# Kernel optimization log

Measured on AMD Instinct MI355X. Metric: run time of the kernel, lower is better.

The kernel has to match this reference:

```python
import jax, jax.numpy as jnp
import numpy as np

V, E, NH, NL, FF, MAXLEN = 32000, 512, 8, 4, 2048, 80
B, L = 32, 80
EPS = 1e-5


def _ln(x, w, b):
    m = jnp.mean(x, axis=-1, keepdims=True)
    v = jnp.var(x, axis=-1, keepdims=True)
    return (x - m) / jnp.sqrt(v + EPS) * w + b


def _mha(q_in, kv_in, in_w, in_b, out_w, out_b, mask):
    # in_w: [3E, E] packed q/k/v like torch MultiheadAttention
    Bq, Lq, Em = q_in.shape
    Lk = kv_in.shape[1]
    hd = Em // NH
    q = q_in @ in_w[:Em].T + in_b[:Em]
    k = kv_in @ in_w[Em:2 * Em].T + in_b[Em:2 * Em]
    v = kv_in @ in_w[2 * Em:].T + in_b[2 * Em:]
    q = q.reshape(Bq, Lq, NH, hd).transpose(0, 2, 1, 3)
    k = k.reshape(Bq, Lk, NH, hd).transpose(0, 2, 1, 3)
    v = v.reshape(Bq, Lk, NH, hd).transpose(0, 2, 1, 3)
    s = jnp.einsum('bhqd,bhkd->bhqk', q, k) * (1.0 / float(np.sqrt(hd)))
    if mask is not None:
        s = s + mask
    a = jax.nn.softmax(s, axis=-1)
    o = jnp.einsum('bhqk,bhkd->bhqd', a, v).transpose(0, 2, 1, 3).reshape(Bq, Lq, Em)
    return o @ out_w.T + out_b


def _forward(caps, W_in, b_in, pos_emb, sa_in_w, sa_in_b, sa_out_w, sa_out_b,
             ca_in_w, ca_in_b, ca_out_w, ca_out_b, ff1_w, ff1_b, ff2_w, ff2_b,
             ln1_w, ln1_b, ln2_w, ln2_b, ln3_w, ln3_b, out_w, out_b):
    Bc, Lc = caps.shape
    # one-hot encode then dense Linear(vocab -> emb): semantically an embedding gather
    oh = jax.nn.one_hot(caps, V, dtype=jnp.float32)          # [B, L, V]
    x = oh @ W_in.T + b_in + pos_emb[:Lc][None]               # [B, L, E]
    mask = jnp.where(jnp.triu(jnp.ones((Lc, Lc), bool), 1), -jnp.inf, 0.0).astype(jnp.float32)
    mem = jnp.zeros((Bc, 1, E), jnp.float32)
    for i in range(NL):  # post-norm TransformerDecoderLayer (torch default, relu FFN)
        sa = _mha(x, x, sa_in_w[i], sa_in_b[i], sa_out_w[i], sa_out_b[i], mask)
        x = _ln(x + sa, ln1_w[i], ln1_b[i])
        ca = _mha(x, mem, ca_in_w[i], ca_in_b[i], ca_out_w[i], ca_out_b[i], None)
        x = _ln(x + ca, ln2_w[i], ln2_b[i])
        ff = jax.nn.relu(x @ ff1_w[i].T + ff1_b[i]) @ ff2_w[i].T + ff2_b[i]
        x = _ln(x + ff, ln3_w[i], ln3_b[i])
    return x @ out_w.T + out_b                                # [B, L, V]


def setup_inputs() -> dict:
    key = jax.random.key(0)
    ks = jax.random.split(key, 16)
    g = lambda k, shape, s=0.02: jax.random.normal(k, shape, jnp.float32) * s
    caps = jax.random.randint(ks[0], (B, L), 1, V)  # avoid pad_idx=0
    return {
        'caps': caps,
        'W_in': g(ks[1], (E, V)),
        'b_in': jnp.zeros((E,), jnp.float32),
        'pos_emb': g(ks[2], (MAXLEN, E)),
        'sa_in_w': g(ks[3], (NL, 3 * E, E)),
        'sa_in_b': jnp.zeros((NL, 3 * E), jnp.float32),
        'sa_out_w': g(ks[4], (NL, E, E)),
        'sa_out_b': jnp.zeros((NL, E), jnp.float32),
        'ca_in_w': g(ks[5], (NL, 3 * E, E)),
        'ca_in_b': jnp.zeros((NL, 3 * E), jnp.float32),
        'ca_out_w': g(ks[6], (NL, E, E)),
        'ca_out_b': jnp.zeros((NL, E), jnp.float32),
        'ff1_w': g(ks[7], (NL, FF, E)),
        'ff1_b': jnp.zeros((NL, FF), jnp.float32),
        'ff2_w': g(ks[8], (NL, E, FF)),
        'ff2_b': jnp.zeros((NL, E), jnp.float32),
        'ln1_w': jnp.ones((NL, E), jnp.float32),
        'ln1_b': jnp.zeros((NL, E), jnp.float32),
        'ln2_w': jnp.ones((NL, E), jnp.float32),
        'ln2_b': jnp.zeros((NL, E), jnp.float32),
        'ln3_w': jnp.ones((NL, E), jnp.float32),
        'ln3_b': jnp.zeros((NL, E), jnp.float32),
        'out_w': g(ks[9], (V, E)),
        'out_b': jnp.zeros((V,), jnp.float32),
    }


def reference(caps, W_in, b_in, pos_emb, sa_in_w, sa_in_b, sa_out_w, sa_out_b,
              ca_in_w, ca_in_b, ca_out_w, ca_out_b, ff1_w, ff1_b, ff2_w, ff2_b,
              ln1_w, ln1_b, ln2_w, ln2_b, ln3_w, ln3_b, out_w, out_b):
    return _forward(caps, W_in, b_in, pos_emb, sa_in_w, sa_in_b, sa_out_w, sa_out_b,
                    ca_in_w, ca_in_b, ca_out_w, ca_out_b, ff1_w, ff1_b, ff2_w, ff2_b,
                    ln1_w, ln1_b, ln2_w, ln2_b, ln3_w, ln3_b, out_w, out_b)
```

## Files before the change

kernel.cpp:

```cpp
#include <hip/hip_runtime.h>

typedef __attribute__((ext_vector_type(8))) short short8;
typedef __attribute__((ext_vector_type(4))) float floatx4;

__device__ __forceinline__ unsigned short f2bf(float f) {
  union { float f; unsigned int u; } un; un.f = f;
  unsigned int r = un.u + 0x7FFFu + ((un.u >> 16) & 1u);
  return (unsigned short)(r >> 16);
}
__device__ __forceinline__ float bf2f(unsigned short h) {
  union { unsigned int u; float f; } un; un.u = ((unsigned int)h) << 16;
  return un.f;
}

__device__ __forceinline__ void async_ld16(const unsigned short* g, unsigned short* l) {
  __builtin_amdgcn_global_load_lds(
      (const __attribute__((address_space(1))) void*)g,
      (__attribute__((address_space(3))) void*)l, 16, 0, 0);
}

template<int TM, int TN, int OUT_BF16, int RELU>
__global__ __launch_bounds__(256, (TM == 64) ? 4 : 2)
void gemm_bt(const unsigned short* __restrict__ A, const unsigned short* __restrict__ B,
             const float* __restrict__ bias, const float* __restrict__ res,
             void* __restrict__ Cout, int M, int N, int K) {
  constexpr int AELEM = TM * 64;
  constexpr int BELEM = TN * 64;
  constexpr int AIT = AELEM / 2048;
  constexpr int BIT = BELEM / 2048;
  constexpr int FM = TM / 32;
  constexpr int FN = TN / 32;
  __shared__ __align__(16) unsigned short sA[2][AELEM];
  __shared__ __align__(16) unsigned short sB[2][BELEM];
  const int tid = threadIdx.x;
  const int lane = tid & 63;
  const int wave = tid >> 6;
  const int m0 = blockIdx.x * TM;
  const int n0 = blockIdx.y * TN;

  int a_off[AIT], b_off[BIT], lb[AIT > BIT ? AIT : BIT];
#pragma unroll
  for (int it = 0; it < AIT; it++) {
    int e = it * 2048 + tid * 8;
    int r = e >> 6, cb = (e >> 3) & 7;
    a_off[it] = (m0 + r) * K + ((cb ^ (r & 7)) * 8);
    lb[it] = it * 2048 + wave * 512;
  }
#pragma unroll
  for (int it = 0; it < BIT; it++) {
    int e = it * 2048 + tid * 8;
    int r = e >> 6, cb = (e >> 3) & 7;
    b_off[it] = (n0 + r) * K + ((cb ^ (r & 7)) * 8);
  }

  floatx4 acc[FM][FN];
#pragma unroll
  for (int i = 0; i < FM; i++)
#pragma unroll
    for (int j = 0; j < FN; j++) acc[i][j] = (floatx4){0.f, 0.f, 0.f, 0.f};

  const int nkt = K >> 6;
  const int wm = (wave >> 1) * (TM / 2);
  const int wn = (wave & 1) * (TN / 2);
  const int fr = lane & 15;
  const int q = lane >> 4;

  auto stage = [&](int kt, int buf) {
    const int k0 = kt << 6;
#pragma unroll
    for (int it = 0; it < AIT; it++) async_ld16(A + (size_t)a_off[it] + k0, &sA[buf][lb[it]]);
#pragma unroll
    for (int it = 0; it < BIT; it++) async_ld16(B + (size_t)b_off[it] + k0, &sB[buf][lb[it]]);
  };

  stage(0, 0);
  for (int kt = 0; kt < nkt; kt++) {
    __syncthreads();
    if (kt + 1 < nkt) stage(kt + 1, (kt + 1) & 1);
    const unsigned short* pA = sA[kt & 1];
    const unsigned short* pB = sB[kt & 1];
#pragma unroll
    for (int kk = 0; kk < 64; kk += 32) {
      short8 af[FM], bfr[FN];
      const int cba = (kk >> 3) + q;
#pragma unroll
      for (int t = 0; t < FM; t++) {
        int ra = wm + t * 16 + fr;
        af[t] = *(const short8*)&pA[ra * 64 + ((cba ^ (ra & 7)) * 8)];
      }
#pragma unroll
      for (int t = 0; t < FN; t++) {
        int rb = wn + t * 16 + fr;
        bfr[t] = *(const short8*)&pB[rb * 64 + ((cba ^ (rb & 7)) * 8)];
      }
#pragma unroll
      for (int i = 0; i < FM; i++)
#pragma unroll
        for (int j = 0; j < FN; j++)
          acc[i][j] = __builtin_amdgcn_mfma_f32_16x16x32_bf16(af[i], bfr[j], acc[i][j], 0, 0, 0);
    }
  }

#pragma unroll
  for (int i = 0; i < FM; i++) {
#pragma unroll
    for (int j = 0; j < FN; j++) {
#pragma unroll
      for (int rg = 0; rg < 4; rg++) {
        int row = m0 + wm + i * 16 + q * 4 + rg;
        int col = n0 + wn + j * 16 + fr;
        float v = acc[i][j][rg];
        if (bias) v += bias[col];
        if (res)  v += res[(size_t)row * N + col];
        if (RELU) v = v > 0.f ? v : 0.f;
        if (OUT_BF16) ((unsigned short*)Cout)[(size_t)row * N + col] = f2bf(v);
        else          ((float*)Cout)[(size_t)row * N + col] = v;
      }
    }
  }
}

__global__ __launch_bounds__(512)
void embed_kernel(const int* __restrict__ caps, const float* __restrict__ W_in,
                  const float* __restrict__ b_in, const float* __restrict__ pos,
                  float* __restrict__ x, unsigned short* __restrict__ xbf) {
  int pidx = blockIdx.x;
  int l = pidx % 80;
  int tok = caps[pidx];
  int e = threadIdx.x;
  float v = W_in[(size_t)e * 32000 + tok] + b_in[e] + pos[l * 512 + e];
  x[(size_t)pidx * 512 + e] = v;
  xbf[(size_t)pidx * 512 + e] = f2bf(v);
}

__global__ __launch_bounds__(256)
void ln_kernel(const float* __restrict__ in, const float* __restrict__ w,
               const float* __restrict__ b, float* __restrict__ xout,
               unsigned short* __restrict__ xbf) {
  int row = blockIdx.x * 4 + (threadIdx.x >> 6);
  int lane = threadIdx.x & 63;
  const float* p = in + (size_t)row * 512;
  float vals[8];
  float s = 0.f, s2 = 0.f;
#pragma unroll
  for (int j = 0; j < 8; j++) {
    float t = p[lane + j * 64];
    vals[j] = t; s += t; s2 += t * t;
  }
#pragma unroll
  for (int off = 32; off; off >>= 1) { s += __shfl_xor(s, off); s2 += __shfl_xor(s2, off); }
  float mean = s * (1.f / 512.f);
  float inv = rsqrtf(s2 * (1.f / 512.f) - mean * mean + 1e-5f);
#pragma unroll
  for (int j = 0; j < 8; j++) {
    int c = lane + j * 64;
    float y = (vals[j] - mean) * inv * w[c] + b[c];
    xout[(size_t)row * 512 + c] = y;
    xbf[(size_t)row * 512 + c] = f2bf(y);
  }
}

__global__ __launch_bounds__(256)
void ln2x_kernel(const float* __restrict__ in, const float* __restrict__ cav,
                 const float* __restrict__ w1, const float* __restrict__ b1,
                 const float* __restrict__ w2, const float* __restrict__ b2,
                 float* __restrict__ xout, unsigned short* __restrict__ xbf) {
  int row = blockIdx.x * 4 + (threadIdx.x >> 6);
  int lane = threadIdx.x & 63;
  const float* p = in + (size_t)row * 512;
  float vals[8];
  float s = 0.f, s2 = 0.f;
#pragma unroll
  for (int j = 0; j < 8; j++) {
    float t = p[lane + j * 64];
    vals[j] = t; s += t; s2 += t * t;
  }
#pragma unroll
  for (int off = 32; off; off >>= 1) { s += __shfl_xor(s, off); s2 += __shfl_xor(s2, off); }
  float mean = s * (1.f / 512.f);
  float inv = rsqrtf(s2 * (1.f / 512.f) - mean * mean + 1e-5f);
  float s_b = 0.f, s2_b = 0.f;
#pragma unroll
  for (int j = 0; j < 8; j++) {
    int c = lane + j * 64;
    float y = (vals[j] - mean) * inv * w1[c] + b1[c] + cav[c];
    vals[j] = y; s_b += y; s2_b += y * y;
  }
#pragma unroll
  for (int off = 32; off; off >>= 1) { s_b += __shfl_xor(s_b, off); s2_b += __shfl_xor(s2_b, off); }
  float mean2 = s_b * (1.f / 512.f);
  float inv2 = rsqrtf(s2_b * (1.f / 512.f) - mean2 * mean2 + 1e-5f);
#pragma unroll
  for (int j = 0; j < 8; j++) {
    int c = lane + j * 64;
    float y = (vals[j] - mean2) * inv2 * w2[c] + b2[c];
    xout[(size_t)row * 512 + c] = y;
    xbf[(size_t)row * 512 + c] = f2bf(y);
  }
}

__global__ __launch_bounds__(256)
void attn_kernel(const unsigned short* __restrict__ qkv, unsigned short* __restrict__ o) {
  __shared__ __align__(16) unsigned short sq[80][72];
  __shared__ __align__(16) unsigned short sk[80][72];
  __shared__ __align__(16) unsigned short svT[64][96];
  __shared__ __align__(16) unsigned short sp[80][96];
  __shared__ float ss[80][84];
  const int tid = threadIdx.x;
  const int lane = tid & 63;
  const int wave = tid >> 6;
  const int bb = blockIdx.x >> 3, hh = blockIdx.x & 7;
  const unsigned short* base = qkv + (size_t)bb * 80 * 1536 + hh * 64;

  for (int idx = tid; idx < 5120; idx += 256) {
    int r = idx >> 6, c = idx & 63;
    sq[r][c] = base[r * 1536 + c];
    sk[r][c] = base[r * 1536 + 512 + c];
    svT[c][r] = base[r * 1536 + 1024 + c];
  }
  for (int idx = tid; idx < 1024; idx += 256) svT[idx >> 4][80 + (idx & 15)] = 0;
  for (int idx = tid; idx < 1280; idx += 256) sp[idx >> 4][80 + (idx & 15)] = 0;
  __syncthreads();

  const int fr = lane & 15;
  const int q = lane >> 4;

  for (int t = wave; t < 25; t += 4) {
    int i0 = (t / 5) * 16, j0 = (t % 5) * 16;
    floatx4 acc = (floatx4){0.f, 0.f, 0.f, 0.f};
#pragma unroll
    for (int kk = 0; kk < 64; kk += 32) {
      short8 a = *(const short8*)&sq[i0 + fr][kk + q * 8];
      short8 b = *(const short8*)&sk[j0 + fr][kk + q * 8];
      acc = __builtin_amdgcn_mfma_f32_16x16x32_bf16(a, b, acc, 0, 0, 0);
    }
#pragma unroll
    for (int rg = 0; rg < 4; rg++) {
      int row = i0 + q * 4 + rg, col = j0 + fr;
      ss[row][col] = (col <= row) ? acc[rg] * 0.125f : -1e30f;
    }
  }
  __syncthreads();

  if (tid < 80) {
    float mx = -1e30f;
#pragma unroll
    for (int j = 0; j < 80; j++) mx = fmaxf(mx, ss[tid][j]);
    float sum = 0.f;
#pragma unroll
    for (int j = 0; j < 80; j++) { float e = __expf(ss[tid][j] - mx); ss[tid][j] = e; sum += e; }
    float inv = 1.f / sum;
#pragma unroll
    for (int j = 0; j < 80; j++) sp[tid][j] = f2bf(ss[tid][j] * inv);
  }
  __syncthreads();

  for (int t = wave; t < 20; t += 4) {
    int i0 = (t / 4) * 16, d0 = (t % 4) * 16;
    floatx4 acc = (floatx4){0.f, 0.f, 0.f, 0.f};
#pragma unroll
    for (int kk = 0; kk < 96; kk += 32) {
      short8 a = *(const short8*)&sp[i0 + fr][kk + q * 8];
      short8 b = *(const short8*)&svT[d0 + fr][kk + q * 8];
      acc = __builtin_amdgcn_mfma_f32_16x16x32_bf16(a, b, acc, 0, 0, 0);
    }
#pragma unroll
    for (int rg = 0; rg < 4; rg++) {
      int row = i0 + q * 4 + rg;
      o[((size_t)bb * 80 + row) * 512 + hh * 64 + d0 + fr] = f2bf(acc[rg]);
    }
  }
}

__global__ __launch_bounds__(256)
void cavec_kernel(const float* __restrict__ ca_out_w, const float* __restrict__ ca_in_b,
                  const float* __restrict__ ca_out_b, float* __restrict__ cav) {
  int g = blockIdx.x * 4 + (threadIdx.x >> 6);
  int lane = threadIdx.x & 63;
  int l = g >> 9, e = g & 511;
  const float* row = ca_out_w + ((size_t)l * 512 + e) * 512;
  const float* inb = ca_in_b + l * 1536 + 1024;
  float s = 0.f;
#pragma unroll
  for (int j = 0; j < 8; j++) s += row[lane + j * 64] * inb[lane + j * 64];
#pragma unroll
  for (int off = 32; off; off >>= 1) s += __shfl_xor(s, off);
  if (lane == 0) cav[g] = s + ca_out_b[l * 512 + e];
}

__global__ __launch_bounds__(256)
void convert_f2bf(const float* __restrict__ in, unsigned short* __restrict__ out, int n4) {
  int i = blockIdx.x * 256 + threadIdx.x;
  if (i < n4) {
    float4 v = ((const float4*)in)[i];
    ushort4 r;
    r.x = f2bf(v.x); r.y = f2bf(v.y); r.z = f2bf(v.z); r.w = f2bf(v.w);
    ((ushort4*)out)[i] = r;
  }
}

extern "C" void kernel_launch(void* const* d_in, const int* in_sizes, int n_in,
                              void* d_out, int out_size, void* d_ws, size_t ws_size,
                              hipStream_t stream) {
  const int*   caps     = (const int*)d_in[0];
  const float* W_in     = (const float*)d_in[1];
  const float* b_in     = (const float*)d_in[2];
  const float* pos_emb  = (const float*)d_in[3];
  const float* sa_in_w  = (const float*)d_in[4];
  const float* sa_in_b  = (const float*)d_in[5];
  const float* sa_out_w = (const float*)d_in[6];
  const float* sa_out_b = (const float*)d_in[7];
  const float* ca_in_b  = (const float*)d_in[9];
  const float* ca_out_w = (const float*)d_in[10];
  const float* ca_out_b = (const float*)d_in[11];
  const float* ff1_w    = (const float*)d_in[12];
  const float* ff1_b    = (const float*)d_in[13];
  const float* ff2_w    = (const float*)d_in[14];
  const float* ff2_b    = (const float*)d_in[15];
  const float* ln1_w    = (const float*)d_in[16];
  const float* ln1_b    = (const float*)d_in[17];
  const float* ln2_w    = (const float*)d_in[18];
  const float* ln2_b    = (const float*)d_in[19];
  const float* ln3_w    = (const float*)d_in[20];
  const float* ln3_b    = (const float*)d_in[21];
  const float* out_w    = (const float*)d_in[22];
  const float* out_b    = (const float*)d_in[23];

  char* ws = (char*)d_ws;
  size_t off = 0;
  auto alloc = [&](size_t bytes) {
    void* p = ws + off;
    off += (bytes + 255) & ~(size_t)255;
    return p;
  };
  unsigned short* w_sa_in  = (unsigned short*)alloc((size_t)4 * 1536 * 512 * 2);
  unsigned short* w_sa_out = (unsigned short*)alloc((size_t)4 * 512 * 512 * 2);
  unsigned short* w_ff1    = (unsigned short*)alloc((size_t)4 * 2048 * 512 * 2);
  unsigned short* w_ff2    = (unsigned short*)alloc((size_t)4 * 512 * 2048 * 2);
  unsigned short* w_out    = (unsigned short*)alloc((size_t)32000 * 512 * 2);
  float*          x        = (float*)alloc((size_t)2560 * 512 * 4);
  unsigned short* xbf      = (unsigned short*)alloc((size_t)2560 * 512 * 2);
  float*          t        = (float*)alloc((size_t)2560 * 512 * 4);
  unsigned short* qkv      = (unsigned short*)alloc((size_t)2560 * 1536 * 2);
  unsigned short* obf      = (unsigned short*)alloc((size_t)2560 * 512 * 2);
  unsigned short* hbf      = (unsigned short*)alloc((size_t)2560 * 2048 * 2);
  float*          cav      = (float*)alloc((size_t)2048 * 4);

  convert_f2bf<<<(786432 + 255) / 256, 256, 0, stream>>>(sa_in_w, w_sa_in, 786432);
  convert_f2bf<<<(262144 + 255) / 256, 256, 0, stream>>>(sa_out_w, w_sa_out, 262144);
  convert_f2bf<<<(1048576 + 255) / 256, 256, 0, stream>>>(ff1_w, w_ff1, 1048576);
  convert_f2bf<<<(1048576 + 255) / 256, 256, 0, stream>>>(ff2_w, w_ff2, 1048576);
  convert_f2bf<<<(4096000 + 255) / 256, 256, 0, stream>>>(out_w, w_out, 4096000);

  embed_kernel<<<2560, 512, 0, stream>>>(caps, W_in, b_in, pos_emb, x, xbf);
  cavec_kernel<<<512, 256, 0, stream>>>(ca_out_w, ca_in_b, ca_out_b, cav);

  for (int i = 0; i < 4; i++) {
    gemm_bt<128, 128, 1, 0><<<dim3(20, 12), 256, 0, stream>>>(
        xbf, w_sa_in + (size_t)i * 1536 * 512, sa_in_b + i * 1536, nullptr,
        qkv, 2560, 1536, 512);
    attn_kernel<<<256, 256, 0, stream>>>(qkv, obf);
    gemm_bt<64, 64, 0, 0><<<dim3(40, 8), 256, 0, stream>>>(
        obf, w_sa_out + (size_t)i * 512 * 512, sa_out_b + i * 512, x,
        t, 2560, 512, 512);
    ln2x_kernel<<<640, 256, 0, stream>>>(t, cav + i * 512,
        ln1_w + i * 512, ln1_b + i * 512, ln2_w + i * 512, ln2_b + i * 512, x, xbf);
    gemm_bt<128, 128, 1, 1><<<dim3(20, 16), 256, 0, stream>>>(
        xbf, w_ff1 + (size_t)i * 2048 * 512, ff1_b + i * 2048, nullptr,
        hbf, 2560, 2048, 512);
    gemm_bt<64, 64, 0, 0><<<dim3(40, 8), 256, 0, stream>>>(
        hbf, w_ff2 + (size_t)i * 512 * 2048, ff2_b + i * 512, x,
        t, 2560, 512, 2048);
    ln_kernel<<<640, 256, 0, stream>>>(t, ln3_w + i * 512, ln3_b + i * 512, x, xbf);
  }

  gemm_bt<128, 128, 0, 0><<<dim3(20, 250), 256, 0, stream>>>(
      xbf, w_out, out_b, nullptr, (float*)d_out, 2560, 32000, 512);
}
```

Measured before the change: 1.120 ms.

## Triple-buffer GEMM loads, remap blocks per XCD, nontemporal logits stores

The GEMM moves from double to triple buffering of LDS tiles. Explicit vmcnt waits and barriers let two future k-tiles be in flight while the current one is computed. Workgroup IDs are remapped so that consecutive tiles land on the same XCD for better L2 reuse. The large fp32 vocab projection output is written with nontemporal stores to avoid polluting cache. The cost is more LDS per block, and launch_bounds occupancy hints are lowered to match.

```diff
diff --git a/kernel.cpp b/kernel.cpp
--- a/kernel.cpp
+++ b/kernel.cpp
@@ -19,8 +19,8 @@
       (__attribute__((address_space(3))) void*)l, 16, 0, 0);
 }
 
-template<int TM, int TN, int OUT_BF16, int RELU>
-__global__ __launch_bounds__(256, (TM == 64) ? 4 : 2)
+template<int TM, int TN, int OUT_BF16, int RELU, int NT>
+__global__ __launch_bounds__(256, (TM == 64) ? 3 : 1)
 void gemm_bt(const unsigned short* __restrict__ A, const unsigned short* __restrict__ B,
              const float* __restrict__ bias, const float* __restrict__ res,
              void* __restrict__ Cout, int M, int N, int K) {
@@ -28,15 +28,24 @@
   constexpr int BELEM = TN * 64;
   constexpr int AIT = AELEM / 2048;
   constexpr int BIT = BELEM / 2048;
+  constexpr int LPS = AIT + BIT;
   constexpr int FM = TM / 32;
   constexpr int FN = TN / 32;
-  __shared__ __align__(16) unsigned short sA[2][AELEM];
-  __shared__ __align__(16) unsigned short sB[2][BELEM];
+  __shared__ __align__(16) unsigned short sA[3][AELEM];
+  __shared__ __align__(16) unsigned short sB[3][BELEM];
   const int tid = threadIdx.x;
   const int lane = tid & 63;
   const int wave = tid >> 6;
-  const int m0 = blockIdx.x * TM;
-  const int n0 = blockIdx.y * TN;
+
+  const int gx = gridDim.x;
+  const int nwg = gx * gridDim.y;
+  const int ord = blockIdx.y * gx + blockIdx.x;
+  const int qq = nwg >> 3, rr = nwg & 7;
+  const int xcd = ord & 7, idx = ord >> 3;
+  const int lin = (xcd < rr) ? (xcd * (qq + 1) + idx)
+                             : (rr * (qq + 1) + (xcd - rr) * qq + idx);
+  const int m0 = (lin % gx) * TM;
+  const int n0 = (lin / gx) * TN;
 
   int a_off[AIT], b_off[BIT], lb[AIT > BIT ? AIT : BIT];
 #pragma unroll
@@ -74,11 +83,19 @@
   };
 
   stage(0, 0);
+  if (nkt > 1) stage(1, 1);
+  if (nkt > 2) stage(2, 2);
+
+  int buf = 0;
   for (int kt = 0; kt < nkt; kt++) {
-    __syncthreads();
-    if (kt + 1 < nkt) stage(kt + 1, (kt + 1) & 1);
-    const unsigned short* pA = sA[kt & 1];
-    const unsigned short* pB = sB[kt & 1];
+    const int rem = nkt - 1 - kt;
+    if (rem >= 2)      asm volatile("s_waitcnt vmcnt(%0)" :: "n"(2 * LPS) : "memory");
+    else if (rem == 1) asm volatile("s_waitcnt vmcnt(%0)" :: "n"(LPS) : "memory");
+    else               asm volatile("s_waitcnt vmcnt(0)" ::: "memory");
+    __builtin_amdgcn_s_barrier();
+
+    const unsigned short* pA = sA[buf];
+    const unsigned short* pB = sB[buf];
 #pragma unroll
     for (int kk = 0; kk < 64; kk += 32) {
       short8 af[FM], bfr[FN];
@@ -99,6 +116,11 @@
         for (int j = 0; j < FN; j++)
           acc[i][j] = __builtin_amdgcn_mfma_f32_16x16x32_bf16(af[i], bfr[j], acc[i][j], 0, 0, 0);
     }
+
+    asm volatile("s_waitcnt lgkmcnt(0)" ::: "memory");
+    __builtin_amdgcn_s_barrier();
+    if (kt + 3 < nkt) stage(kt + 3, buf);
+    buf = (buf == 2) ? 0 : buf + 1;
   }
 
 #pragma unroll
@@ -113,8 +135,13 @@
         if (bias) v += bias[col];
         if (res)  v += res[(size_t)row * N + col];
         if (RELU) v = v > 0.f ? v : 0.f;
-        if (OUT_BF16) ((unsigned short*)Cout)[(size_t)row * N + col] = f2bf(v);
-        else          ((float*)Cout)[(size_t)row * N + col] = v;
+        if (OUT_BF16) {
+          ((unsigned short*)Cout)[(size_t)row * N + col] = f2bf(v);
+        } else if (NT) {
+          __builtin_nontemporal_store(v, &((float*)Cout)[(size_t)row * N + col]);
+        } else {
+          ((float*)Cout)[(size_t)row * N + col] = v;
+        }
       }
     }
   }
@@ -356,24 +383,24 @@
   cavec_kernel<<<512, 256, 0, stream>>>(ca_out_w, ca_in_b, ca_out_b, cav);
 
   for (int i = 0; i < 4; i++) {
-    gemm_bt<128, 128, 1, 0><<<dim3(20, 12), 256, 0, stream>>>(
+    gemm_bt<128, 128, 1, 0, 0><<<dim3(20, 12), 256, 0, stream>>>(
         xbf, w_sa_in + (size_t)i * 1536 * 512, sa_in_b + i * 1536, nullptr,
         qkv, 2560, 1536, 512);
     attn_kernel<<<256, 256, 0, stream>>>(qkv, obf);
-    gemm_bt<64, 64, 0, 0><<<dim3(40, 8), 256, 0, stream>>>(
+    gemm_bt<64, 64, 0, 0, 0><<<dim3(40, 8), 256, 0, stream>>>(
         obf, w_sa_out + (size_t)i * 512 * 512, sa_out_b + i * 512, x,
         t, 2560, 512, 512);
     ln2x_kernel<<<640, 256, 0, stream>>>(t, cav + i * 512,
         ln1_w + i * 512, ln1_b + i * 512, ln2_w + i * 512, ln2_b + i * 512, x, xbf);
-    gemm_bt<128, 128, 1, 1><<<dim3(20, 16), 256, 0, stream>>>(
+    gemm_bt<128, 128, 1, 1, 0><<<dim3(20, 16), 256, 0, stream>>>(
         xbf, w_ff1 + (size_t)i * 2048 * 512, ff1_b + i * 2048, nullptr,
         hbf, 2560, 2048, 512);
-    gemm_bt<64, 64, 0, 0><<<dim3(40, 8), 256, 0, stream>>>(
+    gemm_bt<64, 64, 0, 0, 0><<<dim3(40, 8), 256, 0, stream>>>(
         hbf, w_ff2 + (size_t)i * 512 * 2048, ff2_b + i * 512, x,
         t, 2560, 512, 2048);
     ln_kernel<<<640, 256, 0, stream>>>(t, ln3_w + i * 512, ln3_b + i * 512, x, xbf);
   }
 
-  gemm_bt<128, 128, 0, 0><<<dim3(20, 250), 256, 0, stream>>>(
+  gemm_bt<128, 128, 0, 0, 1><<<dim3(20, 250), 256, 0, stream>>>(
       xbf, w_out, out_b, nullptr, (float*)d_out, 2560, 32000, 512);
 }
```

Measured after the change: 1.250 ms. 11.6% more time.
